# Kernel optimization log

Hardware: AMD Instinct MI355X
Metric: run time of the kernel (lower is better)

## Reference

```python
import jax, jax.numpy as jnp
import numpy as np


def to_tb(r, size, base=4):
    # (B, size, size, size) -> (B, (size//base)^3, base, base, base)
    n = size // base
    r = r.reshape(-1, size, size, n, base)
    r = r.transpose(0, 1, 3, 2, 4)
    r = r.reshape(-1, size, n * n, base, base)
    r = r.transpose(0, 2, 1, 3, 4)
    return r.reshape(-1, n ** 3, base, base, base)


def from_tb(r, size, base=4):
    # inverse-ish of to_tb, ends with an extra (0,1,3,2) transpose as in source
    n = size // base
    r = r.reshape(-1, n * n, size, base, base)
    r = r.transpose(0, 2, 1, 3, 4)
    r = r.reshape(-1, size, size, n, base)
    r = r.transpose(0, 1, 3, 2, 4)
    r = r.reshape(-1, size, size, size)
    return r.transpose(0, 1, 3, 2)


def downscale(r, size):
    r = to_tb(r, size)  # base=4
    r = r.sum(axis=(2, 3, 4)) / 64.0
    r = r.reshape(-1, size // 4, size // 4, size // 4)
    return r.transpose(0, 3, 2, 1)


def setup_inputs() -> dict:
    key = jax.random.key(0)
    # (batch=2, level=4, 4, 4, 4^(3*4-2)) with 4*4*1048576 = 256^3 per slice
    x = jax.random.normal(key, (2, 4, 4, 4, 1048576), dtype=jnp.float32)
    return {"x": x}


def reference(x):
    level = x.shape[1]
    xt = jnp.transpose(x, (1, 0, 2, 3, 4))  # (level, batch, 4, 4, ...)
    batch = xt.shape[1]
    d2 = xt.shape[2]
    size_full = 4 ** level
    n3 = (4 ** (level - 1)) ** 3
    ret = []
    for i in range(level):
        r = xt[i]
        r = from_tb(r, size_full, 4 ** i)  # -> (batch, size, size, size)
        for k in range(i):
            r = downscale(r, 4 ** (level - k))
        for _ in range(i):
            r = jnp.tile(r, (1, 4, 4, 4))
        r = to_tb(r, size_full)  # (batch, n3, 4, 4, 4)
        ret.append(r.reshape(-1, n3, 64))
    out = jnp.stack(ret)  # (level, batch, n3, 64)
    out = out.transpose(1, 0, 2, 3).reshape(batch, -1, d2 ** 3)
    return out
```

## Files before the change

kernel.cpp:

```cpp
#include <hip/hip_runtime.h>


__global__ __launch_bounds__(256) void k_l0(const float* __restrict__ in,
                                            float* __restrict__ out) {
    const int b = blockIdx.y;
    const int Y_hi = blockIdx.x >> 6, Z_hi = blockIdx.x & 63;
    const int tid = threadIdx.x;
    __shared__ float lds[16 * 260];
    const float4* in4 = (const float4*)in;
    float4* out4 = (float4*)out;
    const long in_b4 = (long)b * 16777216;
#pragma unroll
    for (int k = 0; k < 4; ++k) {
        int idx = k * 256 + tid;
        int r = idx >> 6;
        int col4 = idx & 63;
        int Y = Y_hi * 4 + (r >> 2), Z = Z_hi * 4 + (r & 3);
        float4 v = in4[in_b4 + (long)Y * 16384 + Z * 64 + col4];
        *(float4*)&lds[r * 260 + col4 * 4] = v;
    }
    __syncthreads();
    const long out_b4 = (long)b * 16777216 + (long)Z_hi * 65536 + Y_hi * 1024;
#pragma unroll
    for (int k = 0; k < 4; ++k) {
        int idx = k * 256 + tid;
        int X = ((idx >> 4) << 2) + ((tid >> 2) & 3);
        int row0 = (tid & 3) * 4;
        float4 v;
        v.x = lds[(row0 + 0) * 260 + X];
        v.y = lds[(row0 + 1) * 260 + X];
        v.z = lds[(row0 + 2) * 260 + X];
        v.w = lds[(row0 + 3) * 260 + X];
        out4[out_b4 + idx] = v;
    }
}

__global__ __launch_bounds__(256) void k_l1_red(const float* __restrict__ in,
                                                float* __restrict__ d1) {
    const int b = blockIdx.y;
    const int tlow = blockIdx.x;
    const int tid = threadIdx.x;
    const float4* in4 = (const float4*)in;
    const long base4 = (long)b * 16777216 + 4194304;
    float acc[4] = {0.f, 0.f, 0.f, 0.f};
    for (int dz = 0; dz < 4; ++dz) {
        long rb = base4 + (long)(dz * 1024 + tlow) * 1024;
#pragma unroll
        for (int k = 0; k < 4; ++k) {
            float4 v = in4[rb + k * 256 + tid];
            acc[k] += v.x + v.y + v.z + v.w;
        }
    }
#pragma unroll
    for (int k = 0; k < 4; ++k) {
        acc[k] += __shfl_xor(acc[k], 4);
        acc[k] += __shfl_xor(acc[k], 8);
    }
    if ((tid & 12) == 0) {
        int yp = tlow >> 4;
        int zp = ((tlow & 15) << 2) + (tid & 3);
#pragma unroll
        for (int k = 0; k < 4; ++k) {
            int xp = k * 16 + (tid >> 4);
            d1[b * 262144 + xp * 4096 + yp * 64 + zp] = acc[k] * (1.0f / 64.0f);
        }
    }
}

__global__ __launch_bounds__(256) void k_l1_bc(const float* __restrict__ d1,
                                               float* __restrict__ out) {
    const int b = blockIdx.y;
    const int tid = threadIdx.x;
    const float4* d14 = (const float4*)d1;
    float4* out4 = (float4*)out;
    const long ob = (long)b * 16777216 + 4194304;
    const int d1b = b * 65536;
#pragma unroll
    for (int k = 0; k < 4; ++k) {
        int o4 = blockIdx.x * 1024 + k * 256 + tid;
        int u = o4 >> 4;
        int Xl = (o4 >> 2) & 3, Yl = o4 & 3;
        int Xh = u & 63, Yh = (u >> 6) & 63, Zh = u >> 12;
        int x = (Xh & 15) * 4 + Xl, y = (Yh & 15) * 4 + Yl;
        out4[ob + o4] = d14[d1b + x * 1024 + y * 16 + (Zh & 15)];
    }
}

__global__ __launch_bounds__(256) void k_l2_red(const float* __restrict__ in,
                                                float* __restrict__ d2) {
    const int b = blockIdx.y;
    const int yp = blockIdx.x >> 4, xp = blockIdx.x & 15;
    const int tid = threadIdx.x;
    const float4* in4 = (const float4*)in;
    const long base4 = (long)b * 16777216 + 2 * 4194304 + yp * 16384 + xp * 1024;
    float acc = 0.f;
    for (int dz = 0; dz < 16; ++dz) {
        long rb = base4 + (long)dz * 262144;
#pragma unroll
        for (int k = 0; k < 4; ++k) {
            float4 v = in4[rb + k * 256 + tid];
            acc += v.x + v.y + v.z + v.w;
        }
    }
    acc += __shfl_xor(acc, 1);
    acc += __shfl_xor(acc, 2);
    __shared__ float red[64];
    if ((tid & 3) == 0) red[tid >> 2] = acc;
    __syncthreads();
    if (tid < 16) {
        float s = red[tid] + red[16 + tid] + red[32 + tid] + red[48 + tid];
        d2[b * 4096 + xp * 256 + yp * 16 + tid] = s * (1.0f / 4096.0f);
    }
}

__global__ __launch_bounds__(256) void k_l2_bc(const float* __restrict__ d2,
                                               float* __restrict__ out) {
    const int b = blockIdx.y;
    const int tid = threadIdx.x;
    __shared__ float4 tab[1024];
    const float4* d24 = (const float4*)d2;
#pragma unroll
    for (int j = 0; j < 4; ++j) tab[j * 256 + tid] = d24[b * 1024 + j * 256 + tid];
    __syncthreads();
    float4* out4 = (float4*)out;
    const long ob = (long)b * 16777216 + 2 * 4194304;
#pragma unroll
    for (int k = 0; k < 4; ++k) {
        int o4 = blockIdx.x * 1024 + k * 256 + tid;
        int u = o4 >> 4;
        int Xl = (o4 >> 2) & 3, Yl = o4 & 3;
        int Xh = u & 63, Yh = (u >> 6) & 63, Zh = u >> 12;
        int x = (Xh & 3) * 4 + Xl, y = (Yh & 3) * 4 + Yl;
        out4[ob + o4] = tab[x * 64 + y * 4 + (Zh & 3)];
    }
}

__global__ __launch_bounds__(256) void k_l3_red(const float* __restrict__ in,
                                                float* __restrict__ p3) {
    const int b = blockIdx.y;
    const int bx = blockIdx.x;
    const int xp = bx >> 6, hi = (bx >> 2) & 15, dxg = bx & 3;
    const int tid = threadIdx.x;
    const float4* in4 = (const float4*)in;
    const long base4 = (long)b * 16777216 + 3 * 4194304 +
                       (long)hi * 262144 + xp * 65536 + dxg * 16384;
    float acc = 0.f;
    for (int k = 0; k < 64; ++k) {
        float4 v = in4[base4 + k * 256 + tid];
        acc += v.x + v.y + v.z + v.w;
    }
    acc += __shfl_xor(acc, 1);
    acc += __shfl_xor(acc, 2);
    acc += __shfl_xor(acc, 4);
    acc += __shfl_xor(acc, 8);
    __shared__ float red[16];
    if ((tid & 15) == 0) red[tid >> 4] = acc;
    __syncthreads();
    if (tid < 16)
        p3[((b * 4 + xp) * 64 + (bx & 63)) * 16 + tid] = red[tid];
}

__global__ __launch_bounds__(128) void k_l3_fin(const float* __restrict__ p3,
                                                float* __restrict__ d3) {
    const int tid = threadIdx.x;
    const int b = tid >> 6, xp = (tid >> 4) & 3, c = tid & 15;
    float s = 0.f;
    for (int g = 0; g < 64; ++g) s += p3[((b * 4 + xp) * 64 + g) * 16 + c];
    d3[tid] = s * (1.0f / 262144.0f);
}

__global__ __launch_bounds__(256) void k_l3_bc(const float* __restrict__ d3,
                                               float* __restrict__ out) {
    const int b = blockIdx.y;
    const int tid = threadIdx.x;
    const float4* d34 = (const float4*)d3;
    const float4 v = d34[b * 16 + (tid & 15)];
    float4* out4 = (float4*)out;
    const long ob = (long)b * 16777216 + 3 * 4194304;
#pragma unroll
    for (int k = 0; k < 4; ++k)
        out4[ob + blockIdx.x * 1024 + k * 256 + tid] = v;
}

extern "C" void kernel_launch(void* const* d_in, const int* in_sizes, int n_in,
                              void* d_out, int out_size, void* d_ws, size_t ws_size,
                              hipStream_t stream) {
    const float* in = (const float*)d_in[0];
    float* out = (float*)d_out;
    float* ws = (float*)d_ws;
    float* d1 = ws;
    float* d2 = ws + 524288;
    float* p3 = ws + 524288 + 8192;
    float* d3 = ws + 524288 + 8192 + 8192;
    dim3 thr(256);
    k_l0    <<<dim3(4096, 2), thr, 0, stream>>>(in, out);
    k_l1_red<<<dim3(1024, 2), thr, 0, stream>>>(in, d1);
    k_l1_bc <<<dim3(4096, 2), thr, 0, stream>>>(d1, out);
    k_l2_red<<<dim3(256, 2),  thr, 0, stream>>>(in, d2);
    k_l2_bc <<<dim3(4096, 2), thr, 0, stream>>>(d2, out);
    k_l3_red<<<dim3(256, 2),  thr, 0, stream>>>(in, p3);
    k_l3_fin<<<1, 128, 0, stream>>>(p3, d3);
    k_l3_bc <<<dim3(4096, 2), thr, 0, stream>>>(d3, out);
}
```

Measured before the change: 212.7 us.

## Merge eight level kernels into two block-range-dispatched stage kernels

Folds the level-0 transpose and the three level reductions into one launch whose blocks branch on blockIdx.x ranges. The three broadcast writers go into a second launch, with the level-3 final reduction folded redundantly into each broadcast block. This cuts launch count and the serialization between small kernels so the reductions can overlap with the bandwidth-heavy level-0 copy. In exchange, each level-3 broadcast block re-reads the small partials buffer, and shared memory is sized for the largest branch.

```diff
diff --git a/kernel.cpp b/kernel.cpp
--- a/kernel.cpp
+++ b/kernel.cpp
@@ -1,185 +1,175 @@
 #include <hip/hip_runtime.h>
 
 
-__global__ __launch_bounds__(256) void k_l0(const float* __restrict__ in,
-                                            float* __restrict__ out) {
+__global__ __launch_bounds__(256) void k_stage1(const float* __restrict__ in,
+                                                float* __restrict__ out,
+                                                float* __restrict__ d1,
+                                                float* __restrict__ d2,
+                                                float* __restrict__ p3) {
     const int b = blockIdx.y;
-    const int Y_hi = blockIdx.x >> 6, Z_hi = blockIdx.x & 63;
+    const int bx = blockIdx.x;
     const int tid = threadIdx.x;
-    __shared__ float lds[16 * 260];
+    __shared__ float smem[16 * 260];
     const float4* in4 = (const float4*)in;
-    float4* out4 = (float4*)out;
-    const long in_b4 = (long)b * 16777216;
+
+    if (bx < 4096) {
+        const int Y_hi = bx >> 6, Z_hi = bx & 63;
+        float4* out4 = (float4*)out;
+        const long in_b4 = (long)b * 16777216;
 #pragma unroll
-    for (int k = 0; k < 4; ++k) {
-        int idx = k * 256 + tid;
-        int r = idx >> 6;
-        int col4 = idx & 63;
-        int Y = Y_hi * 4 + (r >> 2), Z = Z_hi * 4 + (r & 3);
-        float4 v = in4[in_b4 + (long)Y * 16384 + Z * 64 + col4];
-        *(float4*)&lds[r * 260 + col4 * 4] = v;
-    }
-    __syncthreads();
-    const long out_b4 = (long)b * 16777216 + (long)Z_hi * 65536 + Y_hi * 1024;
+        for (int k = 0; k < 4; ++k) {
+            int idx = k * 256 + tid;
+            int r = idx >> 6;
+            int col4 = idx & 63;
+            int Y = Y_hi * 4 + (r >> 2), Z = Z_hi * 4 + (r & 3);
+            float4 v = in4[in_b4 + (long)Y * 16384 + Z * 64 + col4];
+            *(float4*)&smem[r * 260 + col4 * 4] = v;
+        }
+        __syncthreads();
+        const long out_b4 = (long)b * 16777216 + (long)Z_hi * 65536 + Y_hi * 1024;
 #pragma unroll
-    for (int k = 0; k < 4; ++k) {
-        int idx = k * 256 + tid;
-        int X = ((idx >> 4) << 2) + ((tid >> 2) & 3);
-        int row0 = (tid & 3) * 4;
-        float4 v;
-        v.x = lds[(row0 + 0) * 260 + X];
-        v.y = lds[(row0 + 1) * 260 + X];
-        v.z = lds[(row0 + 2) * 260 + X];
-        v.w = lds[(row0 + 3) * 260 + X];
-        out4[out_b4 + idx] = v;
+        for (int k = 0; k < 4; ++k) {
+            int idx = k * 256 + tid;
+            int X = ((idx >> 4) << 2) + ((tid >> 2) & 3);
+            int row0 = (tid & 3) * 4;
+            float4 v;
+            v.x = smem[(row0 + 0) * 260 + X];
+            v.y = smem[(row0 + 1) * 260 + X];
+            v.z = smem[(row0 + 2) * 260 + X];
+            v.w = smem[(row0 + 3) * 260 + X];
+            out4[out_b4 + idx] = v;
+        }
+    } else if (bx < 5120) {
+        const int tlow = bx - 4096;
+        const long base4 = (long)b * 16777216 + 4194304;
+        float acc[4] = {0.f, 0.f, 0.f, 0.f};
+        for (int dz = 0; dz < 4; ++dz) {
+            long rb = base4 + (long)(dz * 1024 + tlow) * 1024;
+#pragma unroll
+            for (int k = 0; k < 4; ++k) {
+                float4 v = in4[rb + k * 256 + tid];
+                acc[k] += v.x + v.y + v.z + v.w;
+            }
+        }
+#pragma unroll
+        for (int k = 0; k < 4; ++k) {
+            acc[k] += __shfl_xor(acc[k], 4);
+            acc[k] += __shfl_xor(acc[k], 8);
+        }
+        if ((tid & 12) == 0) {
+            int yp = tlow >> 4;
+            int zp = ((tlow & 15) << 2) + (tid & 3);
+#pragma unroll
+            for (int k = 0; k < 4; ++k) {
+                int xp = k * 16 + (tid >> 4);
+                d1[b * 262144 + xp * 4096 + yp * 64 + zp] = acc[k] * (1.0f / 64.0f);
+            }
+        }
+    } else if (bx < 5376) {
+        const int blk = bx - 5120;
+        const int yp = blk >> 4, xp = blk & 15;
+        const long base4 = (long)b * 16777216 + 2 * 4194304 + yp * 16384 + xp * 1024;
+        float acc = 0.f;
+        for (int dz = 0; dz < 16; ++dz) {
+            long rb = base4 + (long)dz * 262144;
+#pragma unroll
+            for (int k = 0; k < 4; ++k) {
+                float4 v = in4[rb + k * 256 + tid];
+                acc += v.x + v.y + v.z + v.w;
+            }
+        }
+        acc += __shfl_xor(acc, 1);
+        acc += __shfl_xor(acc, 2);
+        float* red = smem;
+        if ((tid & 3) == 0) red[tid >> 2] = acc;
+        __syncthreads();
+        if (tid < 16) {
+            float s = red[tid] + red[16 + tid] + red[32 + tid] + red[48 + tid];
+            d2[b * 4096 + xp * 256 + yp * 16 + tid] = s * (1.0f / 4096.0f);
+        }
+    } else {
+        const int blk = bx - 5376;
+        const int xp = blk >> 6, hi = (blk >> 2) & 15, dxg = blk & 3;
+        const long base4 = (long)b * 16777216 + 3 * 4194304 +
+                           (long)hi * 262144 + xp * 65536 + dxg * 16384;
+        float acc = 0.f;
+        for (int k = 0; k < 64; ++k) {
+            float4 v = in4[base4 + k * 256 + tid];
+            acc += v.x + v.y + v.z + v.w;
+        }
+        acc += __shfl_xor(acc, 1);
+        acc += __shfl_xor(acc, 2);
+        acc += __shfl_xor(acc, 4);
+        acc += __shfl_xor(acc, 8);
+        float* red = smem;
+        if ((tid & 15) == 0) red[tid >> 4] = acc;
+        __syncthreads();
+        if (tid < 16)
+            p3[((b * 4 + xp) * 64 + (blk & 63)) * 16 + tid] = red[tid];
     }
 }
 
-__global__ __launch_bounds__(256) void k_l1_red(const float* __restrict__ in,
-                                                float* __restrict__ d1) {
+__global__ __launch_bounds__(256) void k_stage2(const float* __restrict__ d1,
+                                                const float* __restrict__ d2,
+                                                const float* __restrict__ p3,
+                                                float* __restrict__ out) {
     const int b = blockIdx.y;
-    const int tlow = blockIdx.x;
+    const int bx = blockIdx.x;
     const int tid = threadIdx.x;
-    const float4* in4 = (const float4*)in;
-    const long base4 = (long)b * 16777216 + 4194304;
-    float acc[4] = {0.f, 0.f, 0.f, 0.f};
-    for (int dz = 0; dz < 4; ++dz) {
-        long rb = base4 + (long)(dz * 1024 + tlow) * 1024;
+    __shared__ float4 smem4[1024];
+    float4* out4 = (float4*)out;
+
+    if (bx < 4096) {
+        const float4* d14 = (const float4*)d1;
+        const long ob = (long)b * 16777216 + 4194304;
+        const int d1b = b * 65536;
 #pragma unroll
         for (int k = 0; k < 4; ++k) {
-            float4 v = in4[rb + k * 256 + tid];
-            acc[k] += v.x + v.y + v.z + v.w;
+            int o4 = bx * 1024 + k * 256 + tid;
+            int u = o4 >> 4;
+            int Xl = (o4 >> 2) & 3, Yl = o4 & 3;
+            int Xh = u & 63, Yh = (u >> 6) & 63, Zh = u >> 12;
+            int x = (Xh & 15) * 4 + Xl, y = (Yh & 15) * 4 + Yl;
+            out4[ob + o4] = d14[d1b + x * 1024 + y * 16 + (Zh & 15)];
         }
-    }
+    } else if (bx < 8192) {
+        const int blk = bx - 4096;
+        const float4* d24 = (const float4*)d2;
 #pragma unroll
-    for (int k = 0; k < 4; ++k) {
-        acc[k] += __shfl_xor(acc[k], 4);
-        acc[k] += __shfl_xor(acc[k], 8);
-    }
-    if ((tid & 12) == 0) {
-        int yp = tlow >> 4;
-        int zp = ((tlow & 15) << 2) + (tid & 3);
+        for (int j = 0; j < 4; ++j) smem4[j * 256 + tid] = d24[b * 1024 + j * 256 + tid];
+        __syncthreads();
+        const long ob = (long)b * 16777216 + 2 * 4194304;
 #pragma unroll
         for (int k = 0; k < 4; ++k) {
-            int xp = k * 16 + (tid >> 4);
-            d1[b * 262144 + xp * 4096 + yp * 64 + zp] = acc[k] * (1.0f / 64.0f);
+            int o4 = blk * 1024 + k * 256 + tid;
+            int u = o4 >> 4;
+            int Xl = (o4 >> 2) & 3, Yl = o4 & 3;
+            int Xh = u & 63, Yh = (u >> 6) & 63, Zh = u >> 12;
+            int x = (Xh & 3) * 4 + Xl, y = (Yh & 3) * 4 + Yl;
+            out4[ob + o4] = smem4[x * 64 + y * 4 + (Zh & 3)];
         }
+    } else {
+        const int blk = bx - 8192;
+        float* red = (float*)smem4;
+        float* tab = red + 256;
+        int o = tid & 63, grp = tid >> 6;
+        int xp = o >> 4, c = o & 15;
+        const float* pb = p3 + (long)((b * 4 + xp) * 64) * 16 + c;
+        float s = 0.f;
+#pragma unroll
+        for (int k = 0; k < 16; ++k) s += pb[(grp * 16 + k) * 16];
+        red[grp * 64 + o] = s;
+        __syncthreads();
+        if (tid < 64)
+            tab[tid] = (red[tid] + red[64 + tid] + red[128 + tid] + red[192 + tid])
+                       * (1.0f / 262144.0f);
+        __syncthreads();
+        const float4 v = *(const float4*)&tab[(tid & 15) * 4];
+        const long ob = (long)b * 16777216 + 3 * 4194304;
+#pragma unroll
+        for (int k = 0; k < 4; ++k)
+            out4[ob + blk * 1024 + k * 256 + tid] = v;
     }
-}
-
-__global__ __launch_bounds__(256) void k_l1_bc(const float* __restrict__ d1,
-                                               float* __restrict__ out) {
-    const int b = blockIdx.y;
-    const int tid = threadIdx.x;
-    const float4* d14 = (const float4*)d1;
-    float4* out4 = (float4*)out;
-    const long ob = (long)b * 16777216 + 4194304;
-    const int d1b = b * 65536;
-#pragma unroll
-    for (int k = 0; k < 4; ++k) {
-        int o4 = blockIdx.x * 1024 + k * 256 + tid;
-        int u = o4 >> 4;
-        int Xl = (o4 >> 2) & 3, Yl = o4 & 3;
-        int Xh = u & 63, Yh = (u >> 6) & 63, Zh = u >> 12;
-        int x = (Xh & 15) * 4 + Xl, y = (Yh & 15) * 4 + Yl;
-        out4[ob + o4] = d14[d1b + x * 1024 + y * 16 + (Zh & 15)];
-    }
-}
-
-__global__ __launch_bounds__(256) void k_l2_red(const float* __restrict__ in,
-                                                float* __restrict__ d2) {
-    const int b = blockIdx.y;
-    const int yp = blockIdx.x >> 4, xp = blockIdx.x & 15;
-    const int tid = threadIdx.x;
-    const float4* in4 = (const float4*)in;
-    const long base4 = (long)b * 16777216 + 2 * 4194304 + yp * 16384 + xp * 1024;
-    float acc = 0.f;
-    for (int dz = 0; dz < 16; ++dz) {
-        long rb = base4 + (long)dz * 262144;
-#pragma unroll
-        for (int k = 0; k < 4; ++k) {
-            float4 v = in4[rb + k * 256 + tid];
-            acc += v.x + v.y + v.z + v.w;
-        }
-    }
-    acc += __shfl_xor(acc, 1);
-    acc += __shfl_xor(acc, 2);
-    __shared__ float red[64];
-    if ((tid & 3) == 0) red[tid >> 2] = acc;
-    __syncthreads();
-    if (tid < 16) {
-        float s = red[tid] + red[16 + tid] + red[32 + tid] + red[48 + tid];
-        d2[b * 4096 + xp * 256 + yp * 16 + tid] = s * (1.0f / 4096.0f);
-    }
-}
-
-__global__ __launch_bounds__(256) void k_l2_bc(const float* __restrict__ d2,
-                                               float* __restrict__ out) {
-    const int b = blockIdx.y;
-    const int tid = threadIdx.x;
-    __shared__ float4 tab[1024];
-    const float4* d24 = (const float4*)d2;
-#pragma unroll
-    for (int j = 0; j < 4; ++j) tab[j * 256 + tid] = d24[b * 1024 + j * 256 + tid];
-    __syncthreads();
-    float4* out4 = (float4*)out;
-    const long ob = (long)b * 16777216 + 2 * 4194304;
-#pragma unroll
-    for (int k = 0; k < 4; ++k) {
-        int o4 = blockIdx.x * 1024 + k * 256 + tid;
-        int u = o4 >> 4;
-        int Xl = (o4 >> 2) & 3, Yl = o4 & 3;
-        int Xh = u & 63, Yh = (u >> 6) & 63, Zh = u >> 12;
-        int x = (Xh & 3) * 4 + Xl, y = (Yh & 3) * 4 + Yl;
-        out4[ob + o4] = tab[x * 64 + y * 4 + (Zh & 3)];
-    }
-}
-
-__global__ __launch_bounds__(256) void k_l3_red(const float* __restrict__ in,
-                                                float* __restrict__ p3) {
-    const int b = blockIdx.y;
-    const int bx = blockIdx.x;
-    const int xp = bx >> 6, hi = (bx >> 2) & 15, dxg = bx & 3;
-    const int tid = threadIdx.x;
-    const float4* in4 = (const float4*)in;
-    const long base4 = (long)b * 16777216 + 3 * 4194304 +
-                       (long)hi * 262144 + xp * 65536 + dxg * 16384;
-    float acc = 0.f;
-    for (int k = 0; k < 64; ++k) {
-        float4 v = in4[base4 + k * 256 + tid];
-        acc += v.x + v.y + v.z + v.w;
-    }
-    acc += __shfl_xor(acc, 1);
-    acc += __shfl_xor(acc, 2);
-    acc += __shfl_xor(acc, 4);
-    acc += __shfl_xor(acc, 8);
-    __shared__ float red[16];
-    if ((tid & 15) == 0) red[tid >> 4] = acc;
-    __syncthreads();
-    if (tid < 16)
-        p3[((b * 4 + xp) * 64 + (bx & 63)) * 16 + tid] = red[tid];
-}
-
-__global__ __launch_bounds__(128) void k_l3_fin(const float* __restrict__ p3,
-                                                float* __restrict__ d3) {
-    const int tid = threadIdx.x;
-    const int b = tid >> 6, xp = (tid >> 4) & 3, c = tid & 15;
-    float s = 0.f;
-    for (int g = 0; g < 64; ++g) s += p3[((b * 4 + xp) * 64 + g) * 16 + c];
-    d3[tid] = s * (1.0f / 262144.0f);
-}
-
-__global__ __launch_bounds__(256) void k_l3_bc(const float* __restrict__ d3,
-                                               float* __restrict__ out) {
-    const int b = blockIdx.y;
-    const int tid = threadIdx.x;
-    const float4* d34 = (const float4*)d3;
-    const float4 v = d34[b * 16 + (tid & 15)];
-    float4* out4 = (float4*)out;
-    const long ob = (long)b * 16777216 + 3 * 4194304;
-#pragma unroll
-    for (int k = 0; k < 4; ++k)
-        out4[ob + blockIdx.x * 1024 + k * 256 + tid] = v;
 }
 
 extern "C" void kernel_launch(void* const* d_in, const int* in_sizes, int n_in,
@@ -191,14 +181,6 @@
     float* d1 = ws;
     float* d2 = ws + 524288;
     float* p3 = ws + 524288 + 8192;
-    float* d3 = ws + 524288 + 8192 + 8192;
-    dim3 thr(256);
-    k_l0    <<<dim3(4096, 2), thr, 0, stream>>>(in, out);
-    k_l1_red<<<dim3(1024, 2), thr, 0, stream>>>(in, d1);
-    k_l1_bc <<<dim3(4096, 2), thr, 0, stream>>>(d1, out);
-    k_l2_red<<<dim3(256, 2),  thr, 0, stream>>>(in, d2);
-    k_l2_bc <<<dim3(4096, 2), thr, 0, stream>>>(d2, out);
-    k_l3_red<<<dim3(256, 2),  thr, 0, stream>>>(in, p3);
-    k_l3_fin<<<1, 128, 0, stream>>>(p3, d3);
-    k_l3_bc <<<dim3(4096, 2), thr, 0, stream>>>(d3, out);
+    k_stage1<<<dim3(5632, 2),  256, 0, stream>>>(in, out, d1, d2, p3);
+    k_stage2<<<dim3(12288, 2), 256, 0, stream>>>(d1, d2, p3, out);
 }
```

After: 230.3 us. 8.3% more time.
